# Optimization experiments

Measured on AMD Instinct MI355X. Metric: run time of the kernel, lower is better.

## Reference

```python
import jax, jax.numpy as jnp
import numpy as np

EPS = 1e-5


def _bn_silu(x, gamma, beta):
    # train-mode BatchNorm2d (biased batch stats over N,H,W) followed by SiLU
    m = jnp.mean(x, axis=(0, 2, 3), keepdims=True)
    v = jnp.var(x, axis=(0, 2, 3), keepdims=True)
    y = gamma[None, :, None, None] * (x - m) * jax.lax.rsqrt(v + EPS) + beta[None, :, None, None]
    return y * jax.nn.sigmoid(y)


def _deform_conv2d(x, offset, w, b):
    # x: [B,C,H,W]; offset: [B,2*9,H,W] as (dy,dx) pairs per 3x3 tap; w: [Co,C,3,3]
    B, C, H, W = x.shape
    Co = w.shape[0]
    off = offset.reshape(B, 9, 2, H, W)
    k = jnp.arange(9)
    ky = (k // 3 - 1).astype(x.dtype)  # kernel tap offsets, pad=1 so centered
    kx = (k % 3 - 1).astype(x.dtype)
    py = jnp.arange(H, dtype=x.dtype)[None, None, :, None] + ky[None, :, None, None] + off[:, :, 0]
    px = jnp.arange(W, dtype=x.dtype)[None, None, None, :] + kx[None, :, None, None] + off[:, :, 1]
    y0 = jnp.floor(py)
    x0 = jnp.floor(px)
    wy1 = py - y0
    wx1 = px - x0
    xf = x.reshape(B, C, H * W)

    def corner(yi, xi, cw):
        # zero-padded bilinear corner: mask out-of-bounds taps via weight
        valid = (yi >= 0) & (yi < H) & (xi >= 0) & (xi < W)
        idx = jnp.clip(yi, 0, H - 1) * W + jnp.clip(xi, 0, W - 1)
        g = jnp.take_along_axis(xf, idx.reshape(B, 1, -1), axis=2).reshape(B, C, 9, H, W)
        return g * (cw * valid.astype(x.dtype))[:, None]

    y0i = y0.astype(jnp.int32)
    x0i = x0.astype(jnp.int32)
    s = corner(y0i, x0i, (1 - wy1) * (1 - wx1))
    s = s + corner(y0i, x0i + 1, (1 - wy1) * wx1)
    s = s + corner(y0i + 1, x0i, wy1 * (1 - wx1))
    s = s + corner(y0i + 1, x0i + 1, wy1 * wx1)
    out = jnp.einsum('bckhw,ock->bohw', s, w.reshape(Co, C, 9))
    return out + b[None, :, None, None]


def _conv_transpose(x, w, stride, pad):
    # torch ConvTranspose2d: weight layout [Cin, Cout, kh, kw]
    k = w.shape[2]
    wf = jnp.flip(w, (2, 3)).transpose(1, 0, 2, 3)  # -> OIHW, spatially flipped
    p = k - 1 - pad
    return jax.lax.conv_general_dilated(
        x, wf, (1, 1), [(p, p), (p, p)], lhs_dilation=(stride, stride),
        dimension_numbers=('NCHW', 'OIHW', 'NCHW'))


def setup_inputs() -> dict:
    key = jax.random.key(0)
    ks = jax.random.split(key, 4)
    B, C, Co, H, W = 16, 256, 256, 32, 32
    r = lambda k, s, sc: jax.random.normal(k, s, jnp.float32) * sc
    return {
        'x': r(ks[0], (B, C, H, W), 1.0),
        'w_off': r(ks[1], (18, C, 3, 3), 0.01),
        'b_off': jnp.zeros((18,), jnp.float32),
        'w_def': r(ks[2], (Co, C, 3, 3), 0.02),
        'b_def': jnp.zeros((Co,), jnp.float32),
        'gamma1': jnp.ones((Co,), jnp.float32),
        'beta1': jnp.zeros((Co,), jnp.float32),
        'w_dc': r(ks[3], (Co, Co, 4, 4), 0.02),
        'gamma2': jnp.ones((Co,), jnp.float32),
        'beta2': jnp.zeros((Co,), jnp.float32),
    }


def reference(x, w_off, b_off, w_def, b_def, gamma1, beta1, w_dc, gamma2, beta2):
    offset = jax.lax.conv_general_dilated(
        x, w_off, (1, 1), [(1, 1), (1, 1)],
        dimension_numbers=('NCHW', 'OIHW', 'NCHW')) + b_off[None, :, None, None]
    y = _deform_conv2d(x, offset, w_def, b_def)
    y = _bn_silu(y, gamma1, beta1)
    y = _conv_transpose(y, w_dc, 2, 1)
    return _bn_silu(y, gamma2, beta2)
```

## Files before the change

kernel.cpp:

```cpp
#include <hip/hip_runtime.h>
#include <math.h>

#ifdef __has_builtin
#if __has_builtin(__builtin_amdgcn_global_load_lds)
#define HAS_GLL 1
#endif
#endif
#ifndef HAS_GLL
#define HAS_GLL 0
#endif

typedef __attribute__((ext_vector_type(8))) short short8v;
typedef __attribute__((ext_vector_type(4))) float float4v;

__device__ __forceinline__ unsigned short f2bf(float f) {
    unsigned int u = __float_as_uint(f);
    u += 0x7fffu + ((u >> 16) & 1u);
    return (unsigned short)(u >> 16);
}

__device__ __forceinline__ float silu(float y) { return y / (1.f + expf(-y)); }

__device__ __forceinline__ void stage1k(const void* gsrc, void* ldsbase) {
#if HAS_GLL
    __builtin_amdgcn_global_load_lds((const __attribute__((address_space(1))) unsigned int*)gsrc,
                                     (__attribute__((address_space(3))) unsigned int*)ldsbase,
                                     16, 0, 0);
#else
    int lane = threadIdx.x & 63;
    *(float4*)((char*)ldsbase + lane * 16) = *(const float4*)gsrc;
#endif
}

__global__ __launch_bounds__(256) void k_prep_xt(const float* __restrict__ x,
                                                 unsigned short* __restrict__ xT) {
    int hw0 = blockIdx.x * 32, c0 = blockIdx.y * 32, b = blockIdx.z;
    int t = threadIdx.x;
    __shared__ unsigned short tl[32][36];
    {
        int c_l = t >> 3, w4 = (t & 7) * 4;
        float4 v = *(const float4*)&x[(size_t)((b * 256 + c0 + c_l) * 1024) + hw0 + w4];
        tl[c_l][w4 + 0] = f2bf(v.x);
        tl[c_l][w4 + 1] = f2bf(v.y);
        tl[c_l][w4 + 2] = f2bf(v.z);
        tl[c_l][w4 + 3] = f2bf(v.w);
    }
    __syncthreads();
    {
        int hw_l = t >> 3, c4 = (t & 7) * 4;
        unsigned int s0 = tl[c4 + 0][hw_l];
        unsigned int s1 = tl[c4 + 1][hw_l];
        unsigned int s2 = tl[c4 + 2][hw_l];
        unsigned int s3 = tl[c4 + 3][hw_l];
        uint2 pk;
        pk.x = s0 | (s1 << 16);
        pk.y = s2 | (s3 << 16);
        *(uint2*)&xT[(size_t)((b * 1024 + hw0 + hw_l) * 256) + c0 + c4] = pk;
    }
}

__global__ void k_prep_aoff(const float* __restrict__ w_off, unsigned short* __restrict__ A2off) {
    int i = blockIdx.x * 256 + threadIdx.x;
    int slot = i & 31;
    int oc = (i >> 5) & 31;
    int rest = i >> 10;
    int tap = rest % 9;
    int cc8 = rest / 9;
    int cgrp = (slot >> 3) ^ ((oc >> 1) & 3);
    int c = cc8 * 32 + (cgrp << 3) + (slot & 7);
    unsigned short v = 0;
    if (oc < 18) v = f2bf(w_off[(size_t)oc * 2304 + c * 9 + tap]);
    A2off[i] = v;
}

__global__ void k_prep_a1(const float* __restrict__ w_def, unsigned short* __restrict__ A1) {
    int i = blockIdx.x * 256 + threadIdx.x;
    A1[i] = f2bf(w_def[i]);
}

__global__ void k_prep_a2(const float* __restrict__ w_dc, unsigned short* __restrict__ A2) {
    int i = blockIdx.x * 256 + threadIdx.x;
    int ci = i & 255;
    int tq = (i >> 8) & 3;
    int co = (i >> 10) & 255;
    int p  = i >> 18;
    int ph = p >> 1, pw = p & 1;
    int ty = tq >> 1, tx = tq & 1;
    int kh = 2 * ty + 1 - ph;
    int kw = 2 * tx + 1 - pw;
    A2[i] = f2bf(w_dc[((ci * 256 + co) * 4 + kh) * 4 + kw]);
}

__global__ __launch_bounds__(256) void k_off_gemm(const unsigned short* __restrict__ A2off,
                                                  const unsigned short* __restrict__ xT,
                                                  const float* __restrict__ b_off,
                                                  float* __restrict__ off) {
    int hp = blockIdx.x, b = blockIdx.y;
    int h0 = hp * 2;
    int t = threadIdx.x;
    int lane = t & 63, wid = t >> 6;
    int l15 = lane & 15, g = lane >> 4;
    int swg = (l15 >> 1) & 3;
    __shared__ __align__(16) unsigned short As[9 * 32 * 32];
    __shared__ __align__(16) unsigned short Bsx[4 * 34 * 32];
    float4v acc[2];
    float4v z = {0.f, 0.f, 0.f, 0.f};
    acc[0] = z; acc[1] = z;

    int pos = wid * 16 + l15;
    int py = pos >> 5, px = pos & 31;

    for (int cc8 = 0; cc8 < 8; ++cc8) {
        __syncthreads();
        for (int idx = t; idx < 1152; idx += 256)
            stage1k(A2off + (size_t)cc8 * 9216 + idx * 8, (char*)As + idx * 16);
        for (int idx = t; idx < 544; idx += 256) {
            int r = idx / 136;
            int rem = idx - r * 136;
            int col = rem >> 2;
            int sgrp = rem & 3;
            int grp = sgrp ^ ((col >> 1) & 3);
            int h = h0 - 1 + r;
            int w = col - 1;
            uint4 v = {0u, 0u, 0u, 0u};
            if (h >= 0 && h < 32 && w >= 0 && w < 32)
                v = *(const uint4*)&xT[(size_t)((b * 1024 + h * 32 + w) * 256) + cc8 * 32 + grp * 8];
            *(uint4*)((char*)Bsx + ((r * 34 + col) << 6) + (sgrp << 4)) = v;
        }
        __syncthreads();
#pragma unroll
        for (int tap = 0; tap < 9; ++tap) {
            int ky = tap / 3, kx = tap - ky * 3;
            int col = px + kx;
            int rowr = py + ky;
            short8v bbf = *(const short8v*)((const char*)Bsx + ((rowr * 34 + col) << 6) +
                                            ((g ^ ((col >> 1) & 3)) << 4));
            short8v a0 = *(const short8v*)((const char*)As + tap * 2048 + l15 * 64 + ((g ^ swg) << 4));
            short8v a1 = *(const short8v*)((const char*)As + tap * 2048 + (16 + l15) * 64 + ((g ^ swg) << 4));
            acc[0] = __builtin_amdgcn_mfma_f32_16x16x32_bf16(a0, bbf, acc[0], 0, 0, 0);
            acc[1] = __builtin_amdgcn_mfma_f32_16x16x32_bf16(a1, bbf, acc[1], 0, 0, 0);
        }
    }
    int h = h0 + py;
#pragma unroll
    for (int r = 0; r < 4; ++r) {
        int oc = g * 4 + r;
        off[((size_t)(b * 18 + oc) << 10) + (h << 5) + px] = acc[0][r] + b_off[oc];
    }
    if (g == 0) {
#pragma unroll
        for (int r = 0; r < 2; ++r) {
            int oc = 16 + r;
            off[((size_t)(b * 18 + oc) << 10) + (h << 5) + px] = acc[1][r] + b_off[oc];
        }
    }
}

__global__ __launch_bounds__(576) void k_sample(const float* __restrict__ x,
                                                const float* __restrict__ off,
                                                unsigned short* __restrict__ S) {
    int cg = blockIdx.x, b = blockIdx.y, half = blockIdx.z;
    int cbase = cg * 8;
    int t = threadIdx.x;
    int k = t >> 6, lane = t & 63;
    __shared__ __align__(16) unsigned int xpl[4 * 1156];
    __shared__ __align__(16) unsigned short sS[72 * 66];

    for (int u = t; u < 1024; u += 576) {
        int p = u >> 8, row = (u >> 3) & 31, cq = (u & 7) << 2;
        const float* src0 = x + ((size_t)(b * 256 + cbase + 2 * p) << 10) + (row << 5) + cq;
        float4 a = *(const float4*)src0;
        float4 c = *(const float4*)(src0 + 1024);
        uint4 pk;
        pk.x = (unsigned int)f2bf(a.x) | ((unsigned int)f2bf(c.x) << 16);
        pk.y = (unsigned int)f2bf(a.y) | ((unsigned int)f2bf(c.y) << 16);
        pk.z = (unsigned int)f2bf(a.z) | ((unsigned int)f2bf(c.z) << 16);
        pk.w = (unsigned int)f2bf(a.w) | ((unsigned int)f2bf(c.w) << 16);
        *(uint4*)&xpl[p * 1156 + row * 36 + cq] = pk;
    }

    int wr_row = t / 9, wr_q = t - wr_row * 9;
    const float* offk0 = off + ((size_t)(b * 18 + 2 * k) << 10);
    const float* offk1 = off + ((size_t)(b * 18 + 2 * k + 1) << 10);
    int ky = k / 3 - 1, kx = k % 3 - 1;
    __syncthreads();

    for (int ci = 0; ci < 8; ++ci) {
        int chunk = half * 8 + ci;
        int pos = chunk * 64 + lane;
        int h = pos >> 5, w = pos & 31;
        float dy = offk0[pos];
        float dx = offk1[pos];
        float py = (float)(h + ky) + dy;
        float px = (float)(w + kx) + dx;
        float fy = floorf(py), fx = floorf(px);
        int y0i = (int)fy, x0i = (int)fx;
        float wy = py - fy, wxf = px - fx;
        float vy0 = (y0i >= 0 && y0i < 32) ? 1.f : 0.f;
        float vy1 = (y0i >= -1 && y0i < 31) ? 1.f : 0.f;
        float vx0 = (x0i >= 0 && x0i < 32) ? 1.f : 0.f;
        float vx1 = (x0i >= -1 && x0i < 31) ? 1.f : 0.f;
        int y0c = min(max(y0i, 0), 31), y1c = min(max(y0i + 1, 0), 31);
        int x0c = min(max(x0i, 0), 31), x1c = min(max(x0i + 1, 0), 31);
        float w00 = (1.f - wy) * (1.f - wxf) * vy0 * vx0;
        float w01 = (1.f - wy) * wxf * vy0 * vx1;
        float w10 = wy * (1.f - wxf) * vy1 * vx0;
        float w11 = wy * wxf * vy1 * vx1;
        int a00 = y0c * 36 + x0c, a01 = y0c * 36 + x1c;
        int a10 = y1c * 36 + x0c, a11 = y1c * 36 + x1c;
#pragma unroll
        for (int p = 0; p < 4; ++p) {
            const unsigned int* pl = xpl + p * 1156;
            unsigned int c00 = pl[a00], c01 = pl[a01], c10 = pl[a10], c11 = pl[a11];
            float e00 = __uint_as_float(c00 << 16), o00 = __uint_as_float(c00 & 0xFFFF0000u);
            float e01 = __uint_as_float(c01 << 16), o01 = __uint_as_float(c01 & 0xFFFF0000u);
            float e10 = __uint_as_float(c10 << 16), o10 = __uint_as_float(c10 & 0xFFFF0000u);
            float e11 = __uint_as_float(c11 << 16), o11 = __uint_as_float(c11 & 0xFFFF0000u);
            float ve = w00 * e00 + w01 * e01 + w10 * e10 + w11 * e11;
            float vo = w00 * o00 + w01 * o01 + w10 * o10 + w11 * o11;
            sS[((2 * p) * 9 + k) * 66 + lane] = f2bf(ve);
            sS[((2 * p + 1) * 9 + k) * 66 + lane] = f2bf(vo);
        }
        __syncthreads();
        {
            int basekc = wr_q * 8;
            unsigned int s0 = sS[(basekc + 0) * 66 + wr_row];
            unsigned int s1 = sS[(basekc + 1) * 66 + wr_row];
            unsigned int s2 = sS[(basekc + 2) * 66 + wr_row];
            unsigned int s3 = sS[(basekc + 3) * 66 + wr_row];
            unsigned int s4 = sS[(basekc + 4) * 66 + wr_row];
            unsigned int s5 = sS[(basekc + 5) * 66 + wr_row];
            unsigned int s6 = sS[(basekc + 6) * 66 + wr_row];
            unsigned int s7 = sS[(basekc + 7) * 66 + wr_row];
            uint4 qv;
            qv.x = s0 | (s1 << 16);
            qv.y = s2 | (s3 << 16);
            qv.z = s4 | (s5 << 16);
            qv.w = s6 | (s7 << 16);
            *(uint4*)(S + (size_t)(b * 1024 + chunk * 64 + wr_row) * 2304 + cg * 72 + wr_q * 8) = qv;
        }
        __syncthreads();
    }
}

__global__ __launch_bounds__(256) void k_gemm1(const unsigned short* __restrict__ A1,
                                               const unsigned short* __restrict__ S,
                                               const float* __restrict__ b_def,
                                               float* __restrict__ y1,
                                               float* __restrict__ pstats1) {
    int nb = blockIdx.x, mb = blockIdx.y;
    int t = threadIdx.x;
    int lane = t & 63, wid = t >> 6;
    int wm = wid >> 1, wn = wid & 1;
    __shared__ __align__(16) unsigned short As[128 * 32];
    __shared__ __align__(16) unsigned short Bs[64 * 32];
    int m0 = mb * 128, n0 = nb * 64;
    float4v acc[4][2];
    float4v z = {0.f, 0.f, 0.f, 0.f};
#pragma unroll
    for (int i = 0; i < 4; ++i) { acc[i][0] = z; acc[i][1] = z; }
    int rQ = lane >> 2;
    int qA = (lane & 3) ^ ((lane >> 3) & 3);
    const unsigned short* gA0 = A1 + (size_t)(m0 + wid * 32 + rQ) * 2304 + qA * 8;
    const unsigned short* gA1 = gA0 + (size_t)16 * 2304;
    const unsigned short* gB0 = S + (size_t)(n0 + wid * 16 + rQ) * 2304 + qA * 8;
    unsigned short* lA0 = As + wid * 32 * 32;
    unsigned short* lA1 = As + (wid * 32 + 16) * 32;
    unsigned short* lB0 = Bs + wid * 16 * 32;
    int g = lane >> 4, l15 = lane & 15;
    int gs = (g ^ ((l15 >> 1) & 3)) << 4;
    for (int s = 0; s < 72; ++s) {
        __syncthreads();
        stage1k(gA0 + s * 32, lA0);
        stage1k(gA1 + s * 32, lA1);
        stage1k(gB0 + s * 32, lB0);
        __syncthreads();
        short8v a[4], bb[2];
#pragma unroll
        for (int mi = 0; mi < 4; ++mi)
            a[mi] = *(const short8v*)((const char*)As + ((wm * 64 + mi * 16 + l15) * 64 + gs));
#pragma unroll
        for (int ni = 0; ni < 2; ++ni)
            bb[ni] = *(const short8v*)((const char*)Bs + ((wn * 32 + ni * 16 + l15) * 64 + gs));
#pragma unroll
        for (int mi = 0; mi < 4; ++mi)
#pragma unroll
            for (int ni = 0; ni < 2; ++ni)
                acc[mi][ni] = __builtin_amdgcn_mfma_f32_16x16x32_bf16(a[mi], bb[ni], acc[mi][ni], 0, 0, 0);
    }
    __syncthreads();
    int b = n0 >> 10;
    int posb = n0 & 1023;
    float* sred  = (float*)As;
    float* s2red = sred + 256;
#pragma unroll
    for (int mi = 0; mi < 4; ++mi) {
#pragma unroll
        for (int r = 0; r < 4; ++r) {
            int co = m0 + wm * 64 + mi * 16 + g * 4 + r;
            float bv = b_def[co];
            float* dst = y1 + ((size_t)(b * 256 + co) << 10) + posb;
            float s = 0.f, s2 = 0.f;
#pragma unroll
            for (int ni = 0; ni < 2; ++ni) {
                float v = acc[mi][ni][r] + bv;
                dst[wn * 32 + ni * 16 + l15] = v;
                s += v;
                s2 += v * v;
            }
#pragma unroll
            for (int m = 8; m >= 1; m >>= 1) {
                s  += __shfl_xor(s, m, 64);
                s2 += __shfl_xor(s2, m, 64);
            }
            if (l15 == 0) {
                int col = wm * 64 + mi * 16 + g * 4 + r;
                sred[col * 2 + wn]  = s;
                s2red[col * 2 + wn] = s2;
            }
        }
    }
    __syncthreads();
    if (t < 128) {
        float s  = sred[t * 2] + sred[t * 2 + 1];
        float s2 = s2red[t * 2] + s2red[t * 2 + 1];
        int ch = m0 + t;
        pstats1[ch * 256 + nb] = s;
        pstats1[65536 + ch * 256 + nb] = s2;
    }
}

__global__ __launch_bounds__(256) void k_gemm2(const unsigned short* __restrict__ A2,
                                               const unsigned short* __restrict__ y1T,
                                               unsigned short* __restrict__ outP,
                                               float* __restrict__ pstats2) {
    int nb = blockIdx.x, mb = blockIdx.y, p = blockIdx.z;
    int ph = p >> 1, pw = p & 1;
    int t = threadIdx.x;
    int lane = t & 63, wid = t >> 6;
    int wm = wid >> 1, wn = wid & 1;
    int l15 = lane & 15, g = lane >> 4;
    __shared__ __align__(16) unsigned short As[2][8192];
    __shared__ __align__(16) unsigned short Bs[2][8192];
    int m0 = mb * 128, n0 = nb * 128;
    int b = n0 >> 10, pos0 = n0 & 1023, oh0 = pos0 >> 5;

    int dtab[4];
#pragma unroll
    for (int tap = 0; tap < 4; ++tap) {
        int ty = tap >> 1, tx = tap & 1;
        int dy = ph ? (1 - ty) : (-ty);
        int dx = pw ? (1 - tx) : (-tx);
        dtab[tap] = (dy * 34 + dx) * 256;
    }
    const unsigned short* srcA[4];
    const unsigned short* srcB[4];
    int dstoff[4];
#pragma unroll
    for (int it = 0; it < 4; ++it) {
        int idx = t + it * 256;
        int r = idx >> 3, s8 = idx & 7, c = s8 ^ (r & 7);
        srcA[it] = A2 + (size_t)(p * 256 + m0 + r) * 1024 + c * 8;
        int ih = oh0 + (r >> 5) + 1;
        int iw = (r & 31) + 1;
        srcB[it] = y1T + ((size_t)(b * 34 + ih) * 34 + iw) * 256 + c * 8;
        dstoff[it] = idx * 8;
    }

    float4v acc[4][4];
    float4v z = {0.f, 0.f, 0.f, 0.f};
#pragma unroll
    for (int i = 0; i < 4; ++i)
#pragma unroll
        for (int j = 0; j < 4; ++j) acc[i][j] = z;

#pragma unroll
    for (int it = 0; it < 4; ++it) {
        stage1k(srcA[it], &As[0][dstoff[it]]);
        stage1k(srcB[it] + dtab[0], &Bs[0][dstoff[it]]);
    }
    __syncthreads();

    for (int step = 0; step < 16; ++step) {
        int cur = step & 1;
        if (step < 15) {
            int ns = step + 1;
            int tap = ns >> 2;
            int koff = ns * 64;
            int boff = dtab[tap] + (ns & 3) * 64;
#pragma unroll
            for (int it = 0; it < 4; ++it) {
                stage1k(srcA[it] + koff, &As[cur ^ 1][dstoff[it]]);
                stage1k(srcB[it] + boff, &Bs[cur ^ 1][dstoff[it]]);
            }
        }
#pragma unroll
        for (int kk = 0; kk < 2; ++kk) {
            short8v a[4], bb[4];
#pragma unroll
            for (int mi = 0; mi < 4; ++mi) {
                int row = wm * 64 + mi * 16 + l15;
                int slot = ((kk << 2) + g) ^ (row & 7);
                a[mi] = *(const short8v*)((const char*)&As[cur][0] + row * 128 + slot * 16);
            }
#pragma unroll
            for (int ni = 0; ni < 4; ++ni) {
                int row = wn * 64 + ni * 16 + l15;
                int slot = ((kk << 2) + g) ^ (row & 7);
                bb[ni] = *(const short8v*)((const char*)&Bs[cur][0] + row * 128 + slot * 16);
            }
#pragma unroll
            for (int mi = 0; mi < 4; ++mi)
#pragma unroll
                for (int ni = 0; ni < 4; ++ni)
                    acc[mi][ni] = __builtin_amdgcn_mfma_f32_16x16x32_bf16(a[mi], bb[ni], acc[mi][ni], 0, 0, 0);
        }
        __syncthreads();
    }
#pragma unroll
    for (int mi = 0; mi < 4; ++mi) {
#pragma unroll
        for (int r = 0; r < 4; ++r) {
            int co = m0 + wm * 64 + mi * 16 + g * 4 + r;
            unsigned short* dst = outP + ((size_t)((p * 16 + b) * 256 + co) << 10) + pos0;
#pragma unroll
            for (int ni = 0; ni < 4; ++ni)
                dst[wn * 64 + ni * 16 + l15] = f2bf(acc[mi][ni][r]);
        }
    }
    float* sred  = (float*)&As[0][0];
    float* s2red = sred + 256;
#pragma unroll
    for (int mi = 0; mi < 4; ++mi) {
#pragma unroll
        for (int r = 0; r < 4; ++r) {
            float s = 0.f, s2 = 0.f;
#pragma unroll
            for (int ni = 0; ni < 4; ++ni) {
                float v = acc[mi][ni][r];
                s += v;
                s2 += v * v;
            }
#pragma unroll
            for (int m = 8; m >= 1; m >>= 1) {
                s  += __shfl_xor(s, m, 64);
                s2 += __shfl_xor(s2, m, 64);
            }
            if (l15 == 0) {
                int col = wm * 64 + mi * 16 + g * 4 + r;
                sred[col * 2 + wn]  = s;
                s2red[col * 2 + wn] = s2;
            }
        }
    }
    __syncthreads();
    if (t < 128) {
        float s  = sred[t * 2] + sred[t * 2 + 1];
        float s2 = s2red[t * 2] + s2red[t * 2 + 1];
        int row = p * 128 + nb;
        int ch = m0 + t;
        pstats2[ch * 512 + row] = s;
        pstats2[131072 + ch * 512 + row] = s2;
    }
}

__global__ __launch_bounds__(256) void k_bnfin_par(const float* __restrict__ pstats, int nparts,
                                                   float n,
                                                   float* __restrict__ mean, float* __restrict__ rstd) {
    int ch = blockIdx.x;
    int t = threadIdx.x;
    float s = 0.f, s2 = 0.f;
    for (int j = t; j < nparts; j += 256) {
        s  += pstats[ch * nparts + j];
        s2 += pstats[256 * nparts + ch * nparts + j];
    }
    __shared__ float rs[256], rs2[256];
    rs[t] = s; rs2[t] = s2;
    __syncthreads();
    for (int d = 128; d > 0; d >>= 1) {
        if (t < d) { rs[t] += rs[t + d]; rs2[t] += rs2[t + d]; }
        __syncthreads();
    }
    if (t == 0) {
        float m = rs[0] / n;
        float var = rs2[0] / n - m * m;
        mean[ch] = m;
        rstd[ch] = rsqrtf(var + 1e-5f);
    }
}

__global__ __launch_bounds__(256) void k_bnsilu_padT(const float* __restrict__ y1,
                                                     const float* __restrict__ mean,
                                                     const float* __restrict__ rstd,
                                                     const float* __restrict__ gamma,
                                                     const float* __restrict__ beta,
                                                     unsigned short* __restrict__ y1T) {
    int py = blockIdx.x, cg = blockIdx.y, b = blockIdx.z;
    int c0 = cg * 32;
    int t = threadIdx.x;
    __shared__ unsigned short tl[32][36];
    {
        int c_l = t >> 3, px4 = (t & 7) * 4;
        int ch = c0 + c_l;
        float m = mean[ch], rs = rstd[ch], ga = gamma[ch], be = beta[ch];
        float4 v = *(const float4*)&y1[(size_t)((b * 256 + ch) << 10) + (py << 5) + px4];
        tl[c_l][px4 + 0] = f2bf(silu(ga * (v.x - m) * rs + be));
        tl[c_l][px4 + 1] = f2bf(silu(ga * (v.y - m) * rs + be));
        tl[c_l][px4 + 2] = f2bf(silu(ga * (v.z - m) * rs + be));
        tl[c_l][px4 + 3] = f2bf(silu(ga * (v.w - m) * rs + be));
    }
    __syncthreads();
    {
        int px = t >> 3, c4 = (t & 7) * 4;
        unsigned int s0 = tl[c4 + 0][px];
        unsigned int s1 = tl[c4 + 1][px];
        unsigned int s2 = tl[c4 + 2][px];
        unsigned int s3 = tl[c4 + 3][px];
        uint2 pk;
        pk.x = s0 | (s1 << 16);
        pk.y = s2 | (s3 << 16);
        *(uint2*)&y1T[((size_t)(b * 34 + py + 1) * 34 + (px + 1)) * 256 + c0 + c4] = pk;
    }
}

__global__ __launch_bounds__(256) void k_bnsilu_out(const unsigned short* __restrict__ outP,
                                                    const float* __restrict__ mean,
                                                    const float* __restrict__ rstd,
                                                    const float* __restrict__ gamma,
                                                    const float* __restrict__ beta,
                                                    float* __restrict__ out) {
    unsigned int i = blockIdx.x * 256 + threadIdx.x;
    int ow4 = i & 15;
    int oh = (i >> 4) & 63;
    int co = (i >> 10) & 255;
    int b  = i >> 18;
    int p0 = (oh & 1) * 2;
    int pos = ((oh >> 1) << 5) + ow4 * 2;
    const unsigned short* pl0 = outP + ((size_t)((p0 * 16 + b) * 256 + co) << 10) + pos;
    const unsigned short* pl1 = pl0 + ((size_t)16 * 256 << 10);
    unsigned int ue = *(const unsigned int*)pl0;
    unsigned int uo = *(const unsigned int*)pl1;
    float ex = __uint_as_float(ue << 16), ey = __uint_as_float(ue & 0xFFFF0000u);
    float ox = __uint_as_float(uo << 16), oy = __uint_as_float(uo & 0xFFFF0000u);
    float m = mean[co], rs = rstd[co], ga = gamma[co], be = beta[co];
    float4 v;
    v.x = silu(ga * (ex - m) * rs + be);
    v.y = silu(ga * (ox - m) * rs + be);
    v.z = silu(ga * (ey - m) * rs + be);
    v.w = silu(ga * (oy - m) * rs + be);
    *(float4*)&out[((size_t)(b * 256 + co) << 12) + (oh << 6) + ow4 * 4] = v;
}

extern "C" void kernel_launch(void* const* d_in, const int* in_sizes, int n_in,
                              void* d_out, int out_size, void* d_ws, size_t ws_size,
                              hipStream_t stream) {
    const float* x      = (const float*)d_in[0];
    const float* w_off  = (const float*)d_in[1];
    const float* b_off  = (const float*)d_in[2];
    const float* w_def  = (const float*)d_in[3];
    const float* b_def  = (const float*)d_in[4];
    const float* gamma1 = (const float*)d_in[5];
    const float* beta1  = (const float*)d_in[6];
    const float* w_dc   = (const float*)d_in[7];
    const float* gamma2 = (const float*)d_in[8];
    const float* beta2  = (const float*)d_in[9];
    float* out = (float*)d_out;

    char* base = (char*)d_ws;
    unsigned short* S    = (unsigned short*)base;
    float*          y1   = (float*)(base + 75497472);
    unsigned short* y1T  = (unsigned short*)(base + 92274688);
    unsigned short* A1   = (unsigned short*)(base + 101744640);
    unsigned short* A2   = (unsigned short*)(base + 102924288);
    float*          off  = (float*)(base + 105021440);
    float*          stats = (float*)(base + 106201088);
    float* mean1 = stats, *rstd1 = stats + 256, *mean2 = stats + 512, *rstd2 = stats + 768;
    float* pstats1 = off;
    float* pstats2 = off;
    unsigned short* xT    = (unsigned short*)base;
    unsigned short* A2off = (unsigned short*)(base + 8388608);
    unsigned short* outP = (unsigned short*)base;

    k_prep_a1<<<2304, 256, 0, stream>>>(w_def, A1);
    k_prep_a2<<<4096, 256, 0, stream>>>(w_dc, A2);
    k_prep_aoff<<<288, 256, 0, stream>>>(w_off, A2off);
    k_prep_xt<<<dim3(32, 8, 16), 256, 0, stream>>>(x, xT);
    k_off_gemm<<<dim3(16, 16), 256, 0, stream>>>(A2off, xT, b_off, off);
    k_sample<<<dim3(32, 16, 2), 576, 0, stream>>>(x, off, S);
    k_gemm1<<<dim3(256, 2), 256, 0, stream>>>(A1, S, b_def, y1, pstats1);
    k_bnfin_par<<<256, 256, 0, stream>>>(pstats1, 256, 16384.f, mean1, rstd1);
    hipMemsetAsync(y1T, 0, 9469952, stream);
    k_bnsilu_padT<<<dim3(32, 8, 16), 256, 0, stream>>>(y1, mean1, rstd1, gamma1, beta1, y1T);
    k_gemm2<<<dim3(128, 2, 4), 256, 0, stream>>>(A2, y1T, outP, pstats2);
    k_bnfin_par<<<256, 256, 0, stream>>>(pstats2, 512, 65536.f, mean2, rstd2);
    k_bnsilu_out<<<16384, 256, 0, stream>>>(outP, mean2, rstd2, gamma2, beta2, out);
}
```

Measured before the change: 205.9 us.

## Double-buffer gemm1 with 64-wide K, fuse prep kernels, write padding in-kernel

```diff
diff --git a/kernel.cpp b/kernel.cpp
--- a/kernel.cpp
+++ b/kernel.cpp
@@ -32,63 +32,69 @@
 #endif
 }
 
-__global__ __launch_bounds__(256) void k_prep_xt(const float* __restrict__ x,
-                                                 unsigned short* __restrict__ xT) {
-    int hw0 = blockIdx.x * 32, c0 = blockIdx.y * 32, b = blockIdx.z;
+__global__ __launch_bounds__(256) void k_prep_all(const float* __restrict__ w_def,
+                                                  const float* __restrict__ w_dc,
+                                                  const float* __restrict__ w_off,
+                                                  const float* __restrict__ x,
+                                                  unsigned short* __restrict__ A1,
+                                                  unsigned short* __restrict__ A2,
+                                                  unsigned short* __restrict__ A2off,
+                                                  unsigned short* __restrict__ xT) {
+    int blk = blockIdx.x;
     int t = threadIdx.x;
     __shared__ unsigned short tl[32][36];
-    {
-        int c_l = t >> 3, w4 = (t & 7) * 4;
-        float4 v = *(const float4*)&x[(size_t)((b * 256 + c0 + c_l) * 1024) + hw0 + w4];
-        tl[c_l][w4 + 0] = f2bf(v.x);
-        tl[c_l][w4 + 1] = f2bf(v.y);
-        tl[c_l][w4 + 2] = f2bf(v.z);
-        tl[c_l][w4 + 3] = f2bf(v.w);
-    }
-    __syncthreads();
-    {
-        int hw_l = t >> 3, c4 = (t & 7) * 4;
-        unsigned int s0 = tl[c4 + 0][hw_l];
-        unsigned int s1 = tl[c4 + 1][hw_l];
-        unsigned int s2 = tl[c4 + 2][hw_l];
-        unsigned int s3 = tl[c4 + 3][hw_l];
-        uint2 pk;
-        pk.x = s0 | (s1 << 16);
-        pk.y = s2 | (s3 << 16);
-        *(uint2*)&xT[(size_t)((b * 1024 + hw0 + hw_l) * 256) + c0 + c4] = pk;
-    }
-}
-
-__global__ void k_prep_aoff(const float* __restrict__ w_off, unsigned short* __restrict__ A2off) {
-    int i = blockIdx.x * 256 + threadIdx.x;
-    int slot = i & 31;
-    int oc = (i >> 5) & 31;
-    int rest = i >> 10;
-    int tap = rest % 9;
-    int cc8 = rest / 9;
-    int cgrp = (slot >> 3) ^ ((oc >> 1) & 3);
-    int c = cc8 * 32 + (cgrp << 3) + (slot & 7);
-    unsigned short v = 0;
-    if (oc < 18) v = f2bf(w_off[(size_t)oc * 2304 + c * 9 + tap]);
-    A2off[i] = v;
-}
-
-__global__ void k_prep_a1(const float* __restrict__ w_def, unsigned short* __restrict__ A1) {
-    int i = blockIdx.x * 256 + threadIdx.x;
-    A1[i] = f2bf(w_def[i]);
-}
-
-__global__ void k_prep_a2(const float* __restrict__ w_dc, unsigned short* __restrict__ A2) {
-    int i = blockIdx.x * 256 + threadIdx.x;
-    int ci = i & 255;
-    int tq = (i >> 8) & 3;
-    int co = (i >> 10) & 255;
-    int p  = i >> 18;
-    int ph = p >> 1, pw = p & 1;
-    int ty = tq >> 1, tx = tq & 1;
-    int kh = 2 * ty + 1 - ph;
-    int kw = 2 * tx + 1 - pw;
-    A2[i] = f2bf(w_dc[((ci * 256 + co) * 4 + kh) * 4 + kw]);
+    if (blk < 4096) {
+        int i = blk * 256 + t;
+        int ci = i & 255;
+        int tq = (i >> 8) & 3;
+        int co = (i >> 10) & 255;
+        int p  = i >> 18;
+        int ph = p >> 1, pw = p & 1;
+        int ty = tq >> 1, tx = tq & 1;
+        int kh = 2 * ty + 1 - ph;
+        int kw = 2 * tx + 1 - pw;
+        A2[i] = f2bf(w_dc[((ci * 256 + co) * 4 + kh) * 4 + kw]);
+    } else if (blk < 6400) {
+        int i = (blk - 4096) * 256 + t;
+        A1[i] = f2bf(w_def[i]);
+    } else if (blk < 6688) {
+        int i = (blk - 6400) * 256 + t;
+        int slot = i & 31;
+        int oc = (i >> 5) & 31;
+        int rest = i >> 10;
+        int tap = rest % 9;
+        int cc8 = rest / 9;
+        int cgrp = (slot >> 3) ^ ((oc >> 1) & 3);
+        int c = cc8 * 32 + (cgrp << 3) + (slot & 7);
+        unsigned short v = 0;
+        if (oc < 18) v = f2bf(w_off[(size_t)oc * 2304 + c * 9 + tap]);
+        A2off[i] = v;
+    } else {
+        int blk2 = blk - 6688;
+        int hw0 = (blk2 & 31) * 32;
+        int c0 = ((blk2 >> 5) & 7) * 32;
+        int b = blk2 >> 8;
+        {
+            int c_l = t >> 3, w4 = (t & 7) * 4;
+            float4 v = *(const float4*)&x[(size_t)((b * 256 + c0 + c_l) * 1024) + hw0 + w4];
+            tl[c_l][w4 + 0] = f2bf(v.x);
+            tl[c_l][w4 + 1] = f2bf(v.y);
+            tl[c_l][w4 + 2] = f2bf(v.z);
+            tl[c_l][w4 + 3] = f2bf(v.w);
+        }
+        __syncthreads();
+        {
+            int hw_l = t >> 3, c4 = (t & 7) * 4;
+            unsigned int s0 = tl[c4 + 0][hw_l];
+            unsigned int s1 = tl[c4 + 1][hw_l];
+            unsigned int s2 = tl[c4 + 2][hw_l];
+            unsigned int s3 = tl[c4 + 3][hw_l];
+            uint2 pk;
+            pk.x = s0 | (s1 << 16);
+            pk.y = s2 | (s3 << 16);
+            *(uint2*)&xT[(size_t)((b * 1024 + hw0 + hw_l) * 256) + c0 + c4] = pk;
+        }
+    }
 }
 
 __global__ __launch_bounds__(256) void k_off_gemm(const unsigned short* __restrict__ A2off,
@@ -252,46 +258,78 @@
     int t = threadIdx.x;
     int lane = t & 63, wid = t >> 6;
     int wm = wid >> 1, wn = wid & 1;
-    __shared__ __align__(16) unsigned short As[128 * 32];
-    __shared__ __align__(16) unsigned short Bs[64 * 32];
+    int l15 = lane & 15, g = lane >> 4;
+    __shared__ __align__(16) unsigned short As[2][8192];
+    __shared__ __align__(16) unsigned short Bs[2][4096];
     int m0 = mb * 128, n0 = nb * 64;
+    int b = n0 >> 10, pos0 = n0 & 1023;
+
+    const unsigned short* srcA[4];
+    int dA[4];
+    const unsigned short* srcB[2];
+    int dB[2];
+#pragma unroll
+    for (int it = 0; it < 4; ++it) {
+        int idx = t + it * 256;
+        int r = idx >> 3, s8 = idx & 7, c = s8 ^ (r & 7);
+        srcA[it] = A1 + (size_t)(m0 + r) * 2304 + c * 8;
+        dA[it] = idx * 8;
+    }
+#pragma unroll
+    for (int it = 0; it < 2; ++it) {
+        int idx = t + it * 256;
+        int r = idx >> 3, s8 = idx & 7, c = s8 ^ (r & 7);
+        srcB[it] = S + (size_t)(n0 + r) * 2304 + c * 8;
+        dB[it] = idx * 8;
+    }
+
     float4v acc[4][2];
     float4v z = {0.f, 0.f, 0.f, 0.f};
 #pragma unroll
     for (int i = 0; i < 4; ++i) { acc[i][0] = z; acc[i][1] = z; }
-    int rQ = lane >> 2;
-    int qA = (lane & 3) ^ ((lane >> 3) & 3);
-    const unsigned short* gA0 = A1 + (size_t)(m0 + wid * 32 + rQ) * 2304 + qA * 8;
-    const unsigned short* gA1 = gA0 + (size_t)16 * 2304;
-    const unsigned short* gB0 = S + (size_t)(n0 + wid * 16 + rQ) * 2304 + qA * 8;
-    unsigned short* lA0 = As + wid * 32 * 32;
-    unsigned short* lA1 = As + (wid * 32 + 16) * 32;
-    unsigned short* lB0 = Bs + wid * 16 * 32;
-    int g = lane >> 4, l15 = lane & 15;
-    int gs = (g ^ ((l15 >> 1) & 3)) << 4;
-    for (int s = 0; s < 72; ++s) {
-        __syncthreads();
-        stage1k(gA0 + s * 32, lA0);
-        stage1k(gA1 + s * 32, lA1);
-        stage1k(gB0 + s * 32, lB0);
-        __syncthreads();
-        short8v a[4], bb[2];
-#pragma unroll
-        for (int mi = 0; mi < 4; ++mi)
-            a[mi] = *(const short8v*)((const char*)As + ((wm * 64 + mi * 16 + l15) * 64 + gs));
-#pragma unroll
-        for (int ni = 0; ni < 2; ++ni)
-            bb[ni] = *(const short8v*)((const char*)Bs + ((wn * 32 + ni * 16 + l15) * 64 + gs));
-#pragma unroll
-        for (int mi = 0; mi < 4; ++mi)
-#pragma unroll
-            for (int ni = 0; ni < 2; ++ni)
-                acc[mi][ni] = __builtin_amdgcn_mfma_f32_16x16x32_bf16(a[mi], bb[ni], acc[mi][ni], 0, 0, 0);
-    }
+
+#pragma unroll
+    for (int it = 0; it < 4; ++it) stage1k(srcA[it], &As[0][dA[it]]);
+#pragma unroll
+    for (int it = 0; it < 2; ++it) stage1k(srcB[it], &Bs[0][dB[it]]);
     __syncthreads();
-    int b = n0 >> 10;
-    int posb = n0 & 1023;
-    float* sred  = (float*)As;
+
+    for (int step = 0; step < 36; ++step) {
+        int cur = step & 1;
+        if (step < 35) {
+            int koff = (step + 1) * 64;
+#pragma unroll
+            for (int it = 0; it < 4; ++it) stage1k(srcA[it] + koff, &As[cur ^ 1][dA[it]]);
+#pragma unroll
+            for (int it = 0; it < 2; ++it) stage1k(srcB[it] + koff, &Bs[cur ^ 1][dB[it]]);
+        }
+        __builtin_amdgcn_s_setprio(1);
+#pragma unroll
+        for (int kk = 0; kk < 2; ++kk) {
+            short8v a[4], bb[2];
+#pragma unroll
+            for (int mi = 0; mi < 4; ++mi) {
+                int row = wm * 64 + mi * 16 + l15;
+                int slot = ((kk << 2) + g) ^ (row & 7);
+                a[mi] = *(const short8v*)((const char*)&As[cur][0] + row * 128 + slot * 16);
+            }
+#pragma unroll
+            for (int ni = 0; ni < 2; ++ni) {
+                int row = wn * 32 + ni * 16 + l15;
+                int slot = ((kk << 2) + g) ^ (row & 7);
+                bb[ni] = *(const short8v*)((const char*)&Bs[cur][0] + row * 128 + slot * 16);
+            }
+#pragma unroll
+            for (int mi = 0; mi < 4; ++mi)
+#pragma unroll
+                for (int ni = 0; ni < 2; ++ni)
+                    acc[mi][ni] = __builtin_amdgcn_mfma_f32_16x16x32_bf16(a[mi], bb[ni], acc[mi][ni], 0, 0, 0);
+        }
+        __builtin_amdgcn_s_setprio(0);
+        __syncthreads();
+    }
+
+    float* sred  = (float*)&As[0][0];
     float* s2red = sred + 256;
 #pragma unroll
     for (int mi = 0; mi < 4; ++mi) {
@@ -299,7 +337,7 @@
         for (int r = 0; r < 4; ++r) {
             int co = m0 + wm * 64 + mi * 16 + g * 4 + r;
             float bv = b_def[co];
-            float* dst = y1 + ((size_t)(b * 256 + co) << 10) + posb;
+            float* dst = y1 + ((size_t)(b * 256 + co) << 10) + pos0;
             float s = 0.f, s2 = 0.f;
 #pragma unroll
             for (int ni = 0; ni < 2; ++ni) {
@@ -381,6 +419,7 @@
     }
     __syncthreads();
 
+#pragma unroll
     for (int step = 0; step < 16; ++step) {
         int cur = step & 1;
         if (step < 15) {
@@ -394,6 +433,7 @@
                 stage1k(srcB[it] + boff, &Bs[cur ^ 1][dstoff[it]]);
             }
         }
+        __builtin_amdgcn_s_setprio(1);
 #pragma unroll
         for (int kk = 0; kk < 2; ++kk) {
             short8v a[4], bb[4];
@@ -415,6 +455,7 @@
                 for (int ni = 0; ni < 4; ++ni)
                     acc[mi][ni] = __builtin_amdgcn_mfma_f32_16x16x32_bf16(a[mi], bb[ni], acc[mi][ni], 0, 0, 0);
         }
+        __builtin_amdgcn_s_setprio(0);
         __syncthreads();
     }
 #pragma unroll
@@ -498,12 +539,21 @@
     int py = blockIdx.x, cg = blockIdx.y, b = blockIdx.z;
     int c0 = cg * 32;
     int t = threadIdx.x;
+    uint2 zz; zz.x = 0u; zz.y = 0u;
+    if (py == 0 || py == 33) {
+        for (int u = t; u < 272; u += 256) {
+            int col = u >> 3, c4 = (u & 7) * 4;
+            *(uint2*)&y1T[((size_t)(b * 34 + py) * 34 + col) * 256 + c0 + c4] = zz;
+        }
+        return;
+    }
     __shared__ unsigned short tl[32][36];
+    int iy = py - 1;
     {
         int c_l = t >> 3, px4 = (t & 7) * 4;
         int ch = c0 + c_l;
         float m = mean[ch], rs = rstd[ch], ga = gamma[ch], be = beta[ch];
-        float4 v = *(const float4*)&y1[(size_t)((b * 256 + ch) << 10) + (py << 5) + px4];
+        float4 v = *(const float4*)&y1[(size_t)((b * 256 + ch) << 10) + (iy << 5) + px4];
         tl[c_l][px4 + 0] = f2bf(silu(ga * (v.x - m) * rs + be));
         tl[c_l][px4 + 1] = f2bf(silu(ga * (v.y - m) * rs + be));
         tl[c_l][px4 + 2] = f2bf(silu(ga * (v.z - m) * rs + be));
@@ -519,7 +569,12 @@
         uint2 pk;
         pk.x = s0 | (s1 << 16);
         pk.y = s2 | (s3 << 16);
-        *(uint2*)&y1T[((size_t)(b * 34 + py + 1) * 34 + (px + 1)) * 256 + c0 + c4] = pk;
+        *(uint2*)&y1T[((size_t)(b * 34 + py) * 34 + (px + 1)) * 256 + c0 + c4] = pk;
+    }
+    if (t < 16) {
+        int col = (t >> 3) ? 33 : 0;
+        int c4 = (t & 7) * 4;
+        *(uint2*)&y1T[((size_t)(b * 34 + py) * 34 + col) * 256 + c0 + c4] = zz;
     }
 }
 
@@ -581,16 +636,12 @@
     unsigned short* A2off = (unsigned short*)(base + 8388608);
     unsigned short* outP = (unsigned short*)base;
 
-    k_prep_a1<<<2304, 256, 0, stream>>>(w_def, A1);
-    k_prep_a2<<<4096, 256, 0, stream>>>(w_dc, A2);
-    k_prep_aoff<<<288, 256, 0, stream>>>(w_off, A2off);
-    k_prep_xt<<<dim3(32, 8, 16), 256, 0, stream>>>(x, xT);
+    k_prep_all<<<10784, 256, 0, stream>>>(w_def, w_dc, w_off, x, A1, A2, A2off, xT);
     k_off_gemm<<<dim3(16, 16), 256, 0, stream>>>(A2off, xT, b_off, off);
     k_sample<<<dim3(32, 16, 2), 576, 0, stream>>>(x, off, S);
     k_gemm1<<<dim3(256, 2), 256, 0, stream>>>(A1, S, b_def, y1, pstats1);
     k_bnfin_par<<<256, 256, 0, stream>>>(pstats1, 256, 16384.f, mean1, rstd1);
-    hipMemsetAsync(y1T, 0, 9469952, stream);
-    k_bnsilu_padT<<<dim3(32, 8, 16), 256, 0, stream>>>(y1, mean1, rstd1, gamma1, beta1, y1T);
+    k_bnsilu_padT<<<dim3(34, 8, 16), 256, 0, stream>>>(y1, mean1, rstd1, gamma1, beta1, y1T);
     k_gemm2<<<dim3(128, 2, 4), 256, 0, stream>>>(A2, y1T, outP, pstats2);
     k_bnfin_par<<<256, 256, 0, stream>>>(pstats2, 512, 65536.f, mean2, rstd2);
     k_bnsilu_out<<<16384, 256, 0, stream>>>(outP, mean2, rstd2, gamma2, beta2, out);
```

Result: faster. 185.4 us (-10.0%).
